# Kernel optimization log

Hardware: AMD Instinct MI355X
Metric: run time of the kernel (lower is better)

The kernel has to match this reference:

```python
import jax, jax.numpy as jnp
import numpy as np


def setup_inputs() -> dict:
    key = jax.random.key(0)
    x = jax.random.normal(key, (256, 128, 2048), dtype=jnp.float32)
    return {"x": x}


def reference(x) -> jnp.ndarray:
    # x: (batch, channels, time)
    # 1) average reference: subtract mean across channels per (batch, time)
    x = x - jnp.mean(x, axis=1, keepdims=True)
    # 2) channel-wise zscore: mean/std over time axis per (batch, channel)
    mean = jnp.mean(x, axis=2, keepdims=True)
    std = jnp.std(x, axis=2, keepdims=True)  # population std (ddof=0), matches np.std
    std = jnp.where(std == 0, jnp.ones_like(std), std)
    return (x - mean) / std
```

## Files before the change

### kernel.cpp

```cpp
#include <hip/hip_runtime.h>


#define B 256
#define C 128
#define T 2048

__launch_bounds__(1024, 1)
__global__ void eeg_pre_kernel(const float* __restrict__ x,
                               float* __restrict__ out) {
    const int b = blockIdx.x;
    const size_t base = (size_t)b * (C * T);
    const float* __restrict__ xb = x + base;
    float* __restrict__ ob = out + base;

    __shared__ float mu[T];

    const int tid = threadIdx.x;

    {
        const float2* __restrict__ xb2 = reinterpret_cast<const float2*>(xb);
        float sx = 0.f, sy = 0.f;
        #pragma unroll 8
        for (int c = 0; c < C; ++c) {
            float2 v = xb2[c * (T / 2) + tid];
            sx += v.x;
            sy += v.y;
        }
        const float invC = 1.0f / (float)C;
        reinterpret_cast<float2*>(mu)[tid] = make_float2(sx * invC, sy * invC);
    }
    __syncthreads();

    const int wave = tid >> 6;
    const int lane = tid & 63;

    const float4* __restrict__ mu4 = reinterpret_cast<const float4*>(mu);
    float4 mv[8];
    #pragma unroll
    for (int j = 0; j < 8; ++j) mv[j] = mu4[lane + j * 64];

    #pragma unroll 1
    for (int ci = 0; ci < C / 16; ++ci) {
        const int c = wave * (C / 16) + ci;
        const float4* __restrict__ xc4 =
            reinterpret_cast<const float4*>(xb + (size_t)c * T);
        float4* __restrict__ oc4 = reinterpret_cast<float4*>(ob + (size_t)c * T);

        float4 v[8];
        float sum = 0.f, sq = 0.f;
        #pragma unroll
        for (int j = 0; j < 8; ++j) {
            float4 xv = xc4[lane + j * 64];
            float y0 = xv.x - mv[j].x;
            float y1 = xv.y - mv[j].y;
            float y2 = xv.z - mv[j].z;
            float y3 = xv.w - mv[j].w;
            v[j] = make_float4(y0, y1, y2, y3);
            sum += (y0 + y1) + (y2 + y3);
            sq  += ((y0 * y0 + y1 * y1) + (y2 * y2 + y3 * y3));
        }

        #pragma unroll
        for (int off = 32; off > 0; off >>= 1) {
            sum += __shfl_down(sum, off, 64);
            sq  += __shfl_down(sq,  off, 64);
        }
        sum = __shfl(sum, 0, 64);
        sq  = __shfl(sq,  0, 64);

        const float invT = 1.0f / (float)T;
        float mean = sum * invT;
        float var = sq * invT - mean * mean;
        var = fmaxf(var, 0.f);
        float sd = sqrtf(var);
        float inv = (sd == 0.f) ? 1.0f : 1.0f / sd;

        #pragma unroll
        for (int j = 0; j < 8; ++j) {
            float4 o;
            o.x = (v[j].x - mean) * inv;
            o.y = (v[j].y - mean) * inv;
            o.z = (v[j].z - mean) * inv;
            o.w = (v[j].w - mean) * inv;
            oc4[lane + j * 64] = o;
        }
    }
}

extern "C" void kernel_launch(void* const* d_in, const int* in_sizes, int n_in,
                              void* d_out, int out_size, void* d_ws, size_t ws_size,
                              hipStream_t stream) {
    const float* x = (const float*)d_in[0];
    float* out = (float*)d_out;
    eeg_pre_kernel<<<B, 1024, 0, stream>>>(x, out);
}
```

Before: 483.4 us.

## Split fused kernel into channel-mean and per-channel zscore kernels

Replaces the single per-batch kernel (256 blocks of 1024 threads) with two launches. The first computes the channel mean per (batch, time) into workspace using many small blocks. The second runs one block per (batch, channel) to compute the zscore. This greatly increases the number of blocks available to hide memory latency. The cost is an extra full read of the input and a round trip for the mean through workspace.

```diff
diff --git a/kernel.cpp b/kernel.cpp
--- a/kernel.cpp
+++ b/kernel.cpp
@@ -5,86 +5,96 @@
 #define C 128
 #define T 2048
 
-__launch_bounds__(1024, 1)
-__global__ void eeg_pre_kernel(const float* __restrict__ x,
-                               float* __restrict__ out) {
-    const int b = blockIdx.x;
-    const size_t base = (size_t)b * (C * T);
-    const float* __restrict__ xb = x + base;
-    float* __restrict__ ob = out + base;
-
-    __shared__ float mu[T];
-
+__launch_bounds__(256)
+__global__ void mu_kernel(const float* __restrict__ x, float* __restrict__ mu) {
+    const int b = blockIdx.y;
+    const int t0 = blockIdx.x * 256;
     const int tid = threadIdx.x;
-
-    {
-        const float2* __restrict__ xb2 = reinterpret_cast<const float2*>(xb);
-        float sx = 0.f, sy = 0.f;
-        #pragma unroll 8
-        for (int c = 0; c < C; ++c) {
-            float2 v = xb2[c * (T / 2) + tid];
-            sx += v.x;
-            sy += v.y;
-        }
-        const float invC = 1.0f / (float)C;
-        reinterpret_cast<float2*>(mu)[tid] = make_float2(sx * invC, sy * invC);
-    }
-    __syncthreads();
-
     const int wave = tid >> 6;
     const int lane = tid & 63;
 
-    const float4* __restrict__ mu4 = reinterpret_cast<const float4*>(mu);
-    float4 mv[8];
+    const float4* __restrict__ xp =
+        reinterpret_cast<const float4*>(x + ((size_t)b * C + wave * 32) * T + t0);
+
+    float4 acc = make_float4(0.f, 0.f, 0.f, 0.f);
+    #pragma unroll 8
+    for (int k = 0; k < 32; ++k) {
+        float4 v = xp[(size_t)k * (T / 4) + lane];
+        acc.x += v.x; acc.y += v.y; acc.z += v.z; acc.w += v.w;
+    }
+
+    __shared__ float4 part[4][64];
+    part[wave][lane] = acc;
+    __syncthreads();
+
+    if (wave == 0) {
+        float4 p0 = part[0][lane], p1 = part[1][lane];
+        float4 p2 = part[2][lane], p3 = part[3][lane];
+        const float invC = 1.0f / (float)C;
+        float4 s;
+        s.x = (p0.x + p1.x + p2.x + p3.x) * invC;
+        s.y = (p0.y + p1.y + p2.y + p3.y) * invC;
+        s.z = (p0.z + p1.z + p2.z + p3.z) * invC;
+        s.w = (p0.w + p1.w + p2.w + p3.w) * invC;
+        reinterpret_cast<float4*>(mu + (size_t)b * T + t0)[lane] = s;
+    }
+}
+
+__launch_bounds__(256)
+__global__ void zscore_kernel(const float* __restrict__ x,
+                              const float* __restrict__ mu,
+                              float* __restrict__ out) {
+    const int bc = blockIdx.x;
+    const int b = bc >> 7;
+    const int tid = threadIdx.x;
+    const int wave = tid >> 6;
+    const int lane = tid & 63;
+
+    const float4* __restrict__ xc = reinterpret_cast<const float4*>(x + (size_t)bc * T);
+    const float4* __restrict__ mc = reinterpret_cast<const float4*>(mu + (size_t)b * T);
+
+    float4 v0 = xc[tid];
+    float4 v1 = xc[tid + 256];
+    float4 m0 = mc[tid];
+    float4 m1 = mc[tid + 256];
+
+    float4 y0, y1;
+    y0.x = v0.x - m0.x; y0.y = v0.y - m0.y; y0.z = v0.z - m0.z; y0.w = v0.w - m0.w;
+    y1.x = v1.x - m1.x; y1.y = v1.y - m1.y; y1.z = v1.z - m1.z; y1.w = v1.w - m1.w;
+
+    float sum = ((y0.x + y0.y) + (y0.z + y0.w)) + ((y1.x + y1.y) + (y1.z + y1.w));
+    float sq  = ((y0.x * y0.x + y0.y * y0.y) + (y0.z * y0.z + y0.w * y0.w))
+              + ((y1.x * y1.x + y1.y * y1.y) + (y1.z * y1.z + y1.w * y1.w));
+
     #pragma unroll
-    for (int j = 0; j < 8; ++j) mv[j] = mu4[lane + j * 64];
+    for (int off = 32; off > 0; off >>= 1) {
+        sum += __shfl_xor(sum, off, 64);
+        sq  += __shfl_xor(sq,  off, 64);
+    }
 
-    #pragma unroll 1
-    for (int ci = 0; ci < C / 16; ++ci) {
-        const int c = wave * (C / 16) + ci;
-        const float4* __restrict__ xc4 =
-            reinterpret_cast<const float4*>(xb + (size_t)c * T);
-        float4* __restrict__ oc4 = reinterpret_cast<float4*>(ob + (size_t)c * T);
+    __shared__ float2 wsum[4];
+    if (lane == 0) wsum[wave] = make_float2(sum, sq);
+    __syncthreads();
 
-        float4 v[8];
-        float sum = 0.f, sq = 0.f;
-        #pragma unroll
-        for (int j = 0; j < 8; ++j) {
-            float4 xv = xc4[lane + j * 64];
-            float y0 = xv.x - mv[j].x;
-            float y1 = xv.y - mv[j].y;
-            float y2 = xv.z - mv[j].z;
-            float y3 = xv.w - mv[j].w;
-            v[j] = make_float4(y0, y1, y2, y3);
-            sum += (y0 + y1) + (y2 + y3);
-            sq  += ((y0 * y0 + y1 * y1) + (y2 * y2 + y3 * y3));
-        }
+    float2 a0 = wsum[0], a1 = wsum[1], a2 = wsum[2], a3 = wsum[3];
+    float tsum = (a0.x + a1.x) + (a2.x + a3.x);
+    float tsq  = (a0.y + a1.y) + (a2.y + a3.y);
 
-        #pragma unroll
-        for (int off = 32; off > 0; off >>= 1) {
-            sum += __shfl_down(sum, off, 64);
-            sq  += __shfl_down(sq,  off, 64);
-        }
-        sum = __shfl(sum, 0, 64);
-        sq  = __shfl(sq,  0, 64);
+    const float invT = 1.0f / (float)T;
+    float mean = tsum * invT;
+    float var = tsq * invT - mean * mean;
+    var = fmaxf(var, 0.f);
+    float sd = sqrtf(var);
+    float inv = (sd == 0.f) ? 1.0f : 1.0f / sd;
 
-        const float invT = 1.0f / (float)T;
-        float mean = sum * invT;
-        float var = sq * invT - mean * mean;
-        var = fmaxf(var, 0.f);
-        float sd = sqrtf(var);
-        float inv = (sd == 0.f) ? 1.0f : 1.0f / sd;
-
-        #pragma unroll
-        for (int j = 0; j < 8; ++j) {
-            float4 o;
-            o.x = (v[j].x - mean) * inv;
-            o.y = (v[j].y - mean) * inv;
-            o.z = (v[j].z - mean) * inv;
-            o.w = (v[j].w - mean) * inv;
-            oc4[lane + j * 64] = o;
-        }
-    }
+    float4* __restrict__ oc = reinterpret_cast<float4*>(out + (size_t)bc * T);
+    float4 o0, o1;
+    o0.x = (y0.x - mean) * inv; o0.y = (y0.y - mean) * inv;
+    o0.z = (y0.z - mean) * inv; o0.w = (y0.w - mean) * inv;
+    o1.x = (y1.x - mean) * inv; o1.y = (y1.y - mean) * inv;
+    o1.z = (y1.z - mean) * inv; o1.w = (y1.w - mean) * inv;
+    oc[tid] = o0;
+    oc[tid + 256] = o1;
 }
 
 extern "C" void kernel_launch(void* const* d_in, const int* in_sizes, int n_in,
@@ -92,5 +102,9 @@
                               hipStream_t stream) {
     const float* x = (const float*)d_in[0];
     float* out = (float*)d_out;
-    eeg_pre_kernel<<<B, 1024, 0, stream>>>(x, out);
+    float* mu = (float*)d_ws;
+
+    dim3 gridA(T / 256, B);
+    mu_kernel<<<gridA, 256, 0, stream>>>(x, mu);
+    zscore_kernel<<<B * C, 256, 0, stream>>>(x, mu, out);
 }
```

Result: no change. 478.9 us (-0.9%).
